# Performance work log

Measured on AMD Instinct MI355X. Metric: run time of the kernel, lower is better.

The kernel has to match this reference:

```python
import jax, jax.numpy as jnp
import numpy as np

EMBED = 1024
HEADS = 16
HEAD_DIM = EMBED // HEADS


def setup_inputs() -> dict:
    key = jax.random.key(0)
    ks = jax.random.split(key, 11)
    B, L, E = 2, 2048, EMBED
    s = 1.0 / np.sqrt(E)
    return {
        "query": jax.random.normal(ks[0], (B, L, E), jnp.float32),
        "key": jax.random.normal(ks[1], (B, L, E), jnp.float32),
        "value": jax.random.normal(ks[2], (B, L, E), jnp.float32),
        "Wq": jax.random.normal(ks[3], (E, E), jnp.float32) * s,
        "bq": jax.random.normal(ks[4], (E,), jnp.float32) * s,
        "Wk": jax.random.normal(ks[5], (E, E), jnp.float32) * s,
        "bk": jax.random.normal(ks[6], (E,), jnp.float32) * s,
        "Wv": jax.random.normal(ks[7], (E, E), jnp.float32) * s,
        "bv": jax.random.normal(ks[8], (E,), jnp.float32) * s,
        "Wo": jax.random.normal(ks[9], (E, E), jnp.float32) * s,
        "bo": jax.random.normal(ks[10], (E,), jnp.float32) * s,
    }


def reference(query, key, value, Wq, bq, Wk, bk, Wv, bv, Wo, bo):
    B, Lq, E = query.shape
    Lk = key.shape[1]
    # Linear projections (torch Linear: x @ W.T + b)
    q = (query @ Wq.T + bq).reshape(B, Lq, HEADS, HEAD_DIM).transpose(0, 2, 1, 3)
    k = (key @ Wk.T + bk).reshape(B, Lk, HEADS, HEAD_DIM).transpose(0, 2, 1, 3)
    v = (value @ Wv.T + bv).reshape(B, Lk, HEADS, HEAD_DIM).transpose(0, 2, 1, 3)
    # NOTE: original scales by sqrt(embed_size), not sqrt(head_dim)
    energy = jnp.einsum("bhqd,bhkd->bhqk", q, k) / jnp.sqrt(jnp.float32(E))
    attn = jax.nn.softmax(energy, axis=-1)
    out = jnp.einsum("bhqk,bhkd->bhqd", attn, v)  # [B,H,Lq,D]
    out = out.transpose(0, 2, 1, 3).reshape(B, Lq, E)
    return out @ Wo.T + bo
```

## Files before the change

kernel.cpp:

```cpp
#include <hip/hip_runtime.h>
#include <hip/hip_bf16.h>


typedef __attribute__((ext_vector_type(4))) float f32x4;
typedef __attribute__((ext_vector_type(16))) float f32x16;
typedef __attribute__((ext_vector_type(8))) short bf16x8;
typedef __attribute__((ext_vector_type(4))) short bf16x4;
typedef __attribute__((ext_vector_type(2))) unsigned int u32x2;

static __device__ __forceinline__ unsigned short f2bf(float f) {
  union { float f; unsigned int u; } a; a.f = f;
  unsigned int u = a.u;
  u += 0x7FFFu + ((u >> 16) & 1u);
  return (unsigned short)(u >> 16);
}

static __device__ __forceinline__ unsigned pack2(float lo, float hi) {
  unsigned a = __float_as_uint(lo) + 0x8000u;
  unsigned b = __float_as_uint(hi) + 0x8000u;
  return __builtin_amdgcn_perm(b, a, 0x07060302);
}

static __device__ __forceinline__ unsigned xchg32(unsigned x) {
  u32x2 r = __builtin_amdgcn_permlane32_swap(x, x, false, false);
  return x ^ r[0] ^ r[1];
}

#define AS1(p) ((const __attribute__((address_space(1))) void*)(p))
#define AS3(p) ((__attribute__((address_space(3))) void*)(p))

__global__ __launch_bounds__(256) void cvt_kernel(
    const float* __restrict__ q, const float* __restrict__ k, const float* __restrict__ v,
    const float* __restrict__ wq, const float* __restrict__ wk, const float* __restrict__ wv,
    const float* __restrict__ wo, short* __restrict__ ws) {
  long i = (long)blockIdx.x * 256 + threadIdx.x;
  long e = i * 8;
  const float* src; long off;
  if (e < 12582912) {
    int s = (int)(e >> 22);
    src = s == 0 ? q : (s == 1 ? k : v);
    off = e & 4194303;
  } else {
    long e2 = e - 12582912;
    int s = (int)(e2 >> 20);
    src = s == 0 ? wq : (s == 1 ? wk : (s == 2 ? wv : wo));
    off = e2 & 1048575;
  }
  f32x4 a = *(const f32x4*)(src + off);
  f32x4 b = *(const f32x4*)(src + off + 4);
  bf16x8 o;
  o[0] = (short)f2bf(a[0]); o[1] = (short)f2bf(a[1]);
  o[2] = (short)f2bf(a[2]); o[3] = (short)f2bf(a[3]);
  o[4] = (short)f2bf(b[0]); o[5] = (short)f2bf(b[1]);
  o[6] = (short)f2bf(b[2]); o[7] = (short)f2bf(b[3]);
  *(bf16x8*)(ws + e) = o;
}

__device__ __forceinline__ void gemm_tile(const short* __restrict__ A, const short* __restrict__ B,
                                          int m0, int n0, f32x4 acc[4][4],
                                          short* As, short* Bs) {
  const int t = threadIdx.x;
  const int lane = t & 63, w = t >> 6;
  const int wr = w >> 1, wc = w & 1;
  const int x = lane & 15, g = lane >> 4;
  const int lr = lane >> 3;
  const int lc = ((lane & 7) ^ lr) * 8;
  const int rswz = (x & 7) * 8;

#pragma unroll
  for (int fm = 0; fm < 4; fm++)
#pragma unroll
    for (int fn = 0; fn < 4; fn++)
#pragma unroll
      for (int r = 0; r < 4; r++) acc[fm][fn][r] = 0.0f;

  for (int k0 = 0; k0 < 1024; k0 += 64) {
    __syncthreads();
#pragma unroll
    for (int i = 0; i < 4; i++) {
      int ch = w * 4 + i;
      const short* ga = A + (long)(m0 + ch * 8 + lr) * 1024 + k0 + lc;
      __builtin_amdgcn_global_load_lds(AS1(ga), AS3(As + ch * 512), 16, 0, 0);
      const short* gb = B + (long)(n0 + ch * 8 + lr) * 1024 + k0 + lc;
      __builtin_amdgcn_global_load_lds(AS1(gb), AS3(Bs + ch * 512), 16, 0, 0);
    }
    __syncthreads();
#pragma unroll
    for (int ks = 0; ks < 2; ks++) {
      bf16x8 af[4], bfv[4];
#pragma unroll
      for (int f = 0; f < 4; f++) {
        int c = (ks * 32 + g * 8) ^ rswz;
        af[f]  = *(const bf16x8*)(As + (wr * 64 + f * 16 + x) * 64 + c);
        bfv[f] = *(const bf16x8*)(Bs + (wc * 64 + f * 16 + x) * 64 + c);
      }
#pragma unroll
      for (int fm = 0; fm < 4; fm++)
#pragma unroll
        for (int fn = 0; fn < 4; fn++)
          acc[fm][fn] = __builtin_amdgcn_mfma_f32_16x16x32_bf16(af[fm], bfv[fn], acc[fm][fn], 0, 0, 0);
    }
  }
}

__global__ __launch_bounds__(256) void proj_kernel(
    const short* __restrict__ Xq, const short* __restrict__ Xk, const short* __restrict__ Xv,
    const short* __restrict__ Wq, const short* __restrict__ Wk, const short* __restrict__ Wv,
    const float* __restrict__ bq, const float* __restrict__ bk, const float* __restrict__ bv,
    short* __restrict__ Qo, short* __restrict__ Ko, short* __restrict__ Vto) {
  __shared__ short As[8192], Bs[8192];
  const int lin = blockIdx.z * 256 + blockIdx.y * 8 + blockIdx.x;
  const int wgid = (lin & 7) * 96 + (lin >> 3);
  const int z = wgid >> 8;
  const int m0 = ((wgid >> 3) & 31) * 128, n0 = (wgid & 7) * 128;
  const short* A = z == 0 ? Xq : (z == 1 ? Xk : Xv);
  const short* B = z == 0 ? Wq : (z == 1 ? Wk : Wv);
  const float* bias = z == 0 ? bq : (z == 1 ? bk : bv);
  f32x4 acc[4][4];
  gemm_tile(A, B, m0, n0, acc, As, Bs);

  const int lane = threadIdx.x & 63, w = threadIdx.x >> 6;
  const int wr = w >> 1, wc = w & 1, x = lane & 15, g = lane >> 4;

  if (z == 0) {
    const float scale = 0.04508422002778f;
#pragma unroll
    for (int fn = 0; fn < 4; fn++) {
      int n = n0 + wc * 64 + fn * 16 + x;
      float bb = bias[n];
      int h = n >> 6, d = n & 63;
#pragma unroll
      for (int fm = 0; fm < 4; fm++) {
        int mb = m0 + wr * 64 + fm * 16 + g * 4;
#pragma unroll
        for (int r = 0; r < 4; r++) {
          int m = mb + r;
          int b = m >> 11, l = m & 2047;
          float val = (acc[fm][fn][r] + bb) * scale;
          Qo[((long)((b * 16 + h) * 2048 + l)) * 64 + d] = (short)f2bf(val);
        }
      }
    }
  } else if (z == 1) {
#pragma unroll
    for (int fn = 0; fn < 4; fn++) {
      int n = n0 + wc * 64 + fn * 16 + x;
      float bb = bias[n];
      int h = n >> 6, d = n & 63;
#pragma unroll
      for (int fm = 0; fm < 4; fm++) {
        int mb = m0 + wr * 64 + fm * 16 + g * 4;
#pragma unroll
        for (int r = 0; r < 4; r++) {
          int m = mb + r;
          int b = m >> 11, kv = m & 2047;
          int ds = d ^ ((kv & 7) << 3);
          Ko[((long)((b * 16 + h) * 2048 + kv)) * 64 + ds] = (short)f2bf(acc[fm][fn][r] + bb);
        }
      }
    }
  } else {
#pragma unroll
    for (int fn = 0; fn < 4; fn++) {
      int n = n0 + wc * 64 + fn * 16 + x;
      float bb = bias[n];
      int h = n >> 6, d = n & 63;
#pragma unroll
      for (int fm = 0; fm < 4; fm++) {
        int mb = m0 + wr * 64 + fm * 16 + g * 4;
        int b = mb >> 11, kvb = mb & 2047;
        bf16x4 pk;
#pragma unroll
        for (int r = 0; r < 4; r++) pk[r] = (short)f2bf(acc[fm][fn][r] + bb);
        int kvs = (kvb & ~63) | ((kvb & 63) ^ ((d & 7) << 3));
        *(bf16x4*)(Vto + ((long)((b * 16 + h) * 64 + d)) * 2048 + kvs) = pk;
      }
    }
  }
}

__global__ __launch_bounds__(256, 2) void attn_kernel(
    const short* __restrict__ Qg, const short* __restrict__ Kg,
    const short* __restrict__ Vtg, short* __restrict__ Og) {
  __shared__ __align__(16) short Kl[2][8192];
  __shared__ __align__(16) short Vl[2][8192];
  const int t = threadIdx.x, w = t >> 6, lane = t & 63;
  const int col = lane & 31, hi = lane >> 5;
  const int lin = blockIdx.y * 16 + blockIdx.x;
  const int wgid = (lin & 7) * 64 + (lin >> 3);
  const int bh = wgid >> 4;
  const int q0 = (wgid & 15) * 128 + w * 32;
  const long hb = (long)bh * 2048 * 64;
  const int swz = (col & 7) * 8;

  bf16x8 qf[4];
#pragma unroll
  for (int ksl = 0; ksl < 4; ksl++)
    qf[ksl] = *(const bf16x8*)(Qg + hb + (long)(q0 + col) * 64 + ksl * 16 + hi * 8);

  f32x16 o0, o1;
#pragma unroll
  for (int i = 0; i < 16; i++) { o0[i] = 0.0f; o1[i] = 0.0f; }
  float l_r = 0.0f;

  auto stage = [&](int buf, int kv0) {
#pragma unroll
    for (int it = 0; it < 4; it++) {
      int cb = it * 256 + w * 64;
      const short* gk = Kg + hb + (long)kv0 * 64 + (cb + lane) * 8;
      __builtin_amdgcn_global_load_lds(AS1(gk), AS3(&Kl[buf][cb * 8]), 16, 0, 0);
      int c = cb + lane;
      const short* gv = Vtg + hb + (long)(c >> 4) * 2048 + kv0 + (c & 15) * 8;
      __builtin_amdgcn_global_load_lds(AS1(gv), AS3(&Vl[buf][cb * 8]), 16, 0, 0);
    }
  };

  stage(0, 0);
  __syncthreads();

  for (int ti = 0; ti < 16; ti++) {
    const int buf = ti & 1;
    if (ti < 15) stage(buf ^ 1, (ti + 1) * 128);

#pragma unroll
    for (int st = 0; st < 2; st++) {
      f32x16 s0, s1;
#pragma unroll
      for (int i = 0; i < 16; i++) { s0[i] = 0.0f; s1[i] = 0.0f; }
      __builtin_amdgcn_s_setprio(1);
#pragma unroll
      for (int ksl = 0; ksl < 4; ksl++) {
        int dcol = (ksl * 16 + hi * 8) ^ swz;
        bf16x8 a0 = *(const bf16x8*)(&Kl[buf][(st * 64 + col) * 64 + dcol]);
        bf16x8 a1 = *(const bf16x8*)(&Kl[buf][(st * 64 + col + 32) * 64 + dcol]);
        s0 = __builtin_amdgcn_mfma_f32_32x32x16_bf16(a0, qf[ksl], s0, 0, 0, 0);
        s1 = __builtin_amdgcn_mfma_f32_32x32x16_bf16(a1, qf[ksl], s1, 0, 0, 0);
      }
      __builtin_amdgcn_s_setprio(0);

#pragma unroll
      for (int i = 0; i < 16; i++) { s0[i] = __builtin_amdgcn_exp2f(s0[i]); }
#pragma unroll
      for (int i = 0; i < 16; i++) { s1[i] = __builtin_amdgcn_exp2f(s1[i]); }
      {
        float a0 = s0[0] + s0[1], a1 = s0[2] + s0[3], a2 = s0[4] + s0[5], a3 = s0[6] + s0[7];
        float a4 = s0[8] + s0[9], a5 = s0[10] + s0[11], a6 = s0[12] + s0[13], a7 = s0[14] + s0[15];
        float b0 = s1[0] + s1[1], b1 = s1[2] + s1[3], b2 = s1[4] + s1[5], b3 = s1[6] + s1[7];
        float b4 = s1[8] + s1[9], b5 = s1[10] + s1[11], b6 = s1[12] + s1[13], b7 = s1[14] + s1[15];
        float c0 = a0 + a1, c1 = a2 + a3, c2 = a4 + a5, c3 = a6 + a7;
        float c4 = b0 + b1, c5 = b2 + b3, c6 = b4 + b5, c7 = b6 + b7;
        float d0 = c0 + c1, d1 = c2 + c3, d2 = c4 + c5, d3 = c6 + c7;
        l_r += (d0 + d1) + (d2 + d3);
      }

#define PVSTEP(SEL, KS)                                                       \
      {                                                                       \
        unsigned pkA0 = pack2(SEL[8 * ((KS) & 1) + 0], SEL[8 * ((KS) & 1) + 1]); \
        unsigned pkA1 = pack2(SEL[8 * ((KS) & 1) + 2], SEL[8 * ((KS) & 1) + 3]); \
        unsigned pkB0 = pack2(SEL[8 * ((KS) & 1) + 4], SEL[8 * ((KS) & 1) + 5]); \
        unsigned pkB1 = pack2(SEL[8 * ((KS) & 1) + 6], SEL[8 * ((KS) & 1) + 7]); \
        unsigned own0 = hi ? pkB0 : pkA0, own1 = hi ? pkB1 : pkA1;            \
        unsigned oth0 = hi ? pkA0 : pkB0, oth1 = hi ? pkA1 : pkB1;            \
        unsigned r0 = xchg32(oth0);                                           \
        unsigned r1 = xchg32(oth1);                                           \
        union { unsigned u[4]; bf16x8 v; } pb;                                \
        pb.u[0] = hi ? r0 : own0; pb.u[1] = hi ? r1 : own1;                   \
        pb.u[2] = hi ? own0 : r0; pb.u[3] = hi ? own1 : r1;                   \
        const int vcol = ((KS) * 16 + hi * 8) ^ swz;                          \
        bf16x8 vb0 = *(const bf16x8*)(&Vl[buf][col * 128 + st * 64 + vcol]);  \
        bf16x8 vb1 = *(const bf16x8*)(&Vl[buf][(col + 32) * 128 + st * 64 + vcol]); \
        __builtin_amdgcn_s_setprio(1);                                        \
        o0 = __builtin_amdgcn_mfma_f32_32x32x16_bf16(vb0, pb.v, o0, 0, 0, 0); \
        o1 = __builtin_amdgcn_mfma_f32_32x32x16_bf16(vb1, pb.v, o1, 0, 0, 0); \
        __builtin_amdgcn_s_setprio(0);                                        \
      }
      PVSTEP(s0, 0)
      PVSTEP(s0, 1)
      PVSTEP(s1, 2)
      PVSTEP(s1, 3)
#undef PVSTEP
    }

    __syncthreads();
  }

  const float l_tot = l_r + __uint_as_float(xchg32(__float_as_uint(l_r)));
  const float inv = 1.0f / l_tot;
  const int b = bh >> 4, h = bh & 15;
  const long base = ((long)(b * 2048 + q0 + col) * 16 + h) * 64;
#pragma unroll
  for (int dh = 0; dh < 2; dh++) {
#pragma unroll
    for (int g2 = 0; g2 < 4; g2++) {
      float x0 = (dh ? o1[g2 * 4 + 0] : o0[g2 * 4 + 0]) * inv;
      float x1 = (dh ? o1[g2 * 4 + 1] : o0[g2 * 4 + 1]) * inv;
      float x2 = (dh ? o1[g2 * 4 + 2] : o0[g2 * 4 + 2]) * inv;
      float x3 = (dh ? o1[g2 * 4 + 3] : o0[g2 * 4 + 3]) * inv;
      u32x2 rr;
      rr[0] = (unsigned)f2bf(x0) | ((unsigned)f2bf(x1) << 16);
      rr[1] = (unsigned)f2bf(x2) | ((unsigned)f2bf(x3) << 16);
      int d = dh * 32 + g2 * 8 + hi * 4;
      *(u32x2*)(Og + base + d) = rr;
    }
  }
}

__global__ __launch_bounds__(256) void out_kernel(
    const short* __restrict__ O, const short* __restrict__ Wo,
    const float* __restrict__ bo, float* __restrict__ out) {
  __shared__ short As[8192], Bs[8192];
  const int lin = blockIdx.y * 8 + blockIdx.x;
  const int wgid = (lin & 7) * 32 + (lin >> 3);
  const int m0 = (wgid >> 3) * 128, n0 = (wgid & 7) * 128;
  f32x4 acc[4][4];
  gemm_tile(O, Wo, m0, n0, acc, As, Bs);
  const int lane = threadIdx.x & 63, w = threadIdx.x >> 6;
  const int wr = w >> 1, wc = w & 1, x = lane & 15, g = lane >> 4;
#pragma unroll
  for (int fn = 0; fn < 4; fn++) {
    int n = n0 + wc * 64 + fn * 16 + x;
    float bb = bo[n];
#pragma unroll
    for (int fm = 0; fm < 4; fm++) {
      int mb = m0 + wr * 64 + fm * 16 + g * 4;
#pragma unroll
      for (int r = 0; r < 4; r++)
        out[(long)(mb + r) * 1024 + n] = acc[fm][fn][r] + bb;
    }
  }
}

extern "C" void kernel_launch(void* const* d_in, const int* in_sizes, int n_in,
                              void* d_out, int out_size, void* d_ws, size_t ws_size,
                              hipStream_t stream) {
  const float* q  = (const float*)d_in[0];
  const float* k  = (const float*)d_in[1];
  const float* v  = (const float*)d_in[2];
  const float* wq = (const float*)d_in[3];
  const float* bq = (const float*)d_in[4];
  const float* wk = (const float*)d_in[5];
  const float* bk = (const float*)d_in[6];
  const float* wv = (const float*)d_in[7];
  const float* bv = (const float*)d_in[8];
  const float* wo = (const float*)d_in[9];
  const float* bo = (const float*)d_in[10];

  short* ws  = (short*)d_ws;
  short* Xq  = ws;
  short* Xk  = Xq + 4194304;
  short* Xv  = Xk + 4194304;
  short* Wqb = Xv + 4194304;
  short* Wkb = Wqb + 1048576;
  short* Wvb = Wkb + 1048576;
  short* Wob = Wvb + 1048576;
  short* Qb  = Wob + 1048576;
  short* Kb  = Qb + 4194304;
  short* Vtb = Kb + 4194304;
  short* Ob  = Vtb + 4194304;

  cvt_kernel<<<8192, 256, 0, stream>>>(q, k, v, wq, wk, wv, wo, ws);
  dim3 gp(8, 32, 3);
  proj_kernel<<<gp, 256, 0, stream>>>(Xq, Xk, Xv, Wqb, Wkb, Wvb, bq, bk, bv, Qb, Kb, Vtb);
  dim3 ga(16, 32);
  attn_kernel<<<ga, 256, 0, stream>>>(Qb, Kb, Vtb, Ob);
  dim3 gf(8, 32);
  out_kernel<<<gf, 256, 0, stream>>>(Ob, Wob, bo, (float*)d_out);
}
```

Baseline: 130.3 us.

## Fuse activation bf16 conversion into projection GEMM and compute row sums via MFMA

The separate conversion pass for the query/key/value activations is removed. The projection GEMM now loads fp32 activations directly, packs them to bf16 in registers and writes them to LDS, which avoids a full write and reread of the activation tensors. In attention, the scalar softmax row-sum reduction is replaced by an extra MFMA against a ones vector that accumulates the denominator. This adds matrix-core work per step and gives up the async global-to-LDS path for the A operand.

Result: no change. 131.8 us (+1.1%).

```diff
diff --git a/kernel.cpp b/kernel.cpp
--- a/kernel.cpp
+++ b/kernel.cpp
@@ -29,23 +29,15 @@
 #define AS1(p) ((const __attribute__((address_space(1))) void*)(p))
 #define AS3(p) ((__attribute__((address_space(3))) void*)(p))
 
-__global__ __launch_bounds__(256) void cvt_kernel(
-    const float* __restrict__ q, const float* __restrict__ k, const float* __restrict__ v,
-    const float* __restrict__ wq, const float* __restrict__ wk, const float* __restrict__ wv,
-    const float* __restrict__ wo, short* __restrict__ ws) {
+__global__ __launch_bounds__(256) void cvtw_kernel(
+    const float* __restrict__ wq, const float* __restrict__ wk,
+    const float* __restrict__ wv, const float* __restrict__ wo,
+    short* __restrict__ ws) {
   long i = (long)blockIdx.x * 256 + threadIdx.x;
   long e = i * 8;
-  const float* src; long off;
-  if (e < 12582912) {
-    int s = (int)(e >> 22);
-    src = s == 0 ? q : (s == 1 ? k : v);
-    off = e & 4194303;
-  } else {
-    long e2 = e - 12582912;
-    int s = (int)(e2 >> 20);
-    src = s == 0 ? wq : (s == 1 ? wk : (s == 2 ? wv : wo));
-    off = e2 & 1048575;
-  }
+  int s = (int)(e >> 20);
+  const float* src = s == 0 ? wq : (s == 1 ? wk : (s == 2 ? wv : wo));
+  long off = e & 1048575;
   f32x4 a = *(const f32x4*)(src + off);
   f32x4 b = *(const f32x4*)(src + off + 4);
   bf16x8 o;
@@ -103,8 +95,69 @@
   }
 }
 
+__device__ __forceinline__ void gemm_tile_f32a(const float* __restrict__ A,
+                                               const short* __restrict__ B,
+                                               int m0, int n0, f32x4 acc[4][4],
+                                               short* As, short* Bs) {
+  const int t = threadIdx.x;
+  const int lane = t & 63, w = t >> 6;
+  const int wr = w >> 1, wc = w & 1;
+  const int x = lane & 15, g = lane >> 4;
+  const int lr = lane >> 3;
+  const int sc = (lane & 7) * 8;
+  const int dcA = sc ^ (lr * 8);
+  const int lcB = ((lane & 7) ^ lr) * 8;
+  const int rswz = (x & 7) * 8;
+
+#pragma unroll
+  for (int fm = 0; fm < 4; fm++)
+#pragma unroll
+    for (int fn = 0; fn < 4; fn++)
+#pragma unroll
+      for (int r = 0; r < 4; r++) acc[fm][fn][r] = 0.0f;
+
+  for (int k0 = 0; k0 < 1024; k0 += 64) {
+    __syncthreads();
+#pragma unroll
+    for (int i = 0; i < 4; i++) {
+      int ch = w * 4 + i;
+      const short* gb = B + (long)(n0 + ch * 8 + lr) * 1024 + k0 + lcB;
+      __builtin_amdgcn_global_load_lds(AS1(gb), AS3(Bs + ch * 512), 16, 0, 0);
+    }
+#pragma unroll
+    for (int i = 0; i < 4; i++) {
+      int ch = w * 4 + i;
+      const float* ga = A + (long)(m0 + ch * 8 + lr) * 1024 + k0 + sc;
+      f32x4 a = *(const f32x4*)ga;
+      f32x4 b2 = *(const f32x4*)(ga + 4);
+      union { unsigned u[4]; bf16x8 v; } pk;
+      pk.u[0] = pack2(a[0], a[1]);
+      pk.u[1] = pack2(a[2], a[3]);
+      pk.u[2] = pack2(b2[0], b2[1]);
+      pk.u[3] = pack2(b2[2], b2[3]);
+      *(bf16x8*)(As + (ch * 8 + lr) * 64 + dcA) = pk.v;
+    }
+    __syncthreads();
+#pragma unroll
+    for (int ks = 0; ks < 2; ks++) {
+      bf16x8 af[4], bfv[4];
+#pragma unroll
+      for (int f = 0; f < 4; f++) {
+        int c = (ks * 32 + g * 8) ^ rswz;
+        af[f]  = *(const bf16x8*)(As + (wr * 64 + f * 16 + x) * 64 + c);
+        bfv[f] = *(const bf16x8*)(Bs + (wc * 64 + f * 16 + x) * 64 + c);
+      }
+#pragma unroll
+      for (int fm = 0; fm < 4; fm++)
+#pragma unroll
+        for (int fn = 0; fn < 4; fn++)
+          acc[fm][fn] = __builtin_amdgcn_mfma_f32_16x16x32_bf16(af[fm], bfv[fn], acc[fm][fn], 0, 0, 0);
+    }
+  }
+}
+
 __global__ __launch_bounds__(256) void proj_kernel(
-    const short* __restrict__ Xq, const short* __restrict__ Xk, const short* __restrict__ Xv,
+    const float* __restrict__ Xq, const float* __restrict__ Xk, const float* __restrict__ Xv,
     const short* __restrict__ Wq, const short* __restrict__ Wk, const short* __restrict__ Wv,
     const float* __restrict__ bq, const float* __restrict__ bk, const float* __restrict__ bv,
     short* __restrict__ Qo, short* __restrict__ Ko, short* __restrict__ Vto) {
@@ -113,11 +166,11 @@
   const int wgid = (lin & 7) * 96 + (lin >> 3);
   const int z = wgid >> 8;
   const int m0 = ((wgid >> 3) & 31) * 128, n0 = (wgid & 7) * 128;
-  const short* A = z == 0 ? Xq : (z == 1 ? Xk : Xv);
+  const float* A = z == 0 ? Xq : (z == 1 ? Xk : Xv);
   const short* B = z == 0 ? Wq : (z == 1 ? Wk : Wv);
   const float* bias = z == 0 ? bq : (z == 1 ? bk : bv);
   f32x4 acc[4][4];
-  gemm_tile(A, B, m0, n0, acc, As, Bs);
+  gemm_tile_f32a(A, B, m0, n0, acc, As, Bs);
 
   const int lane = threadIdx.x & 63, w = threadIdx.x >> 6;
   const int wr = w >> 1, wc = w & 1, x = lane & 15, g = lane >> 4;
@@ -198,10 +251,13 @@
   for (int ksl = 0; ksl < 4; ksl++)
     qf[ksl] = *(const bf16x8*)(Qg + hb + (long)(q0 + col) * 64 + ksl * 16 + hi * 8);
 
-  f32x16 o0, o1;
-#pragma unroll
-  for (int i = 0; i < 16; i++) { o0[i] = 0.0f; o1[i] = 0.0f; }
-  float l_r = 0.0f;
+  union { unsigned u[4]; bf16x8 v; } onesf;
+#pragma unroll
+  for (int i = 0; i < 4; i++) onesf.u[i] = 0x3F803F80u;
+
+  f32x16 o0, o1, o2;
+#pragma unroll
+  for (int i = 0; i < 16; i++) { o0[i] = 0.0f; o1[i] = 0.0f; o2[i] = 0.0f; }
 
   auto stage = [&](int buf, int kv0) {
 #pragma unroll
@@ -242,16 +298,6 @@
       for (int i = 0; i < 16; i++) { s0[i] = __builtin_amdgcn_exp2f(s0[i]); }
 #pragma unroll
       for (int i = 0; i < 16; i++) { s1[i] = __builtin_amdgcn_exp2f(s1[i]); }
-      {
-        float a0 = s0[0] + s0[1], a1 = s0[2] + s0[3], a2 = s0[4] + s0[5], a3 = s0[6] + s0[7];
-        float a4 = s0[8] + s0[9], a5 = s0[10] + s0[11], a6 = s0[12] + s0[13], a7 = s0[14] + s0[15];
-        float b0 = s1[0] + s1[1], b1 = s1[2] + s1[3], b2 = s1[4] + s1[5], b3 = s1[6] + s1[7];
-        float b4 = s1[8] + s1[9], b5 = s1[10] + s1[11], b6 = s1[12] + s1[13], b7 = s1[14] + s1[15];
-        float c0 = a0 + a1, c1 = a2 + a3, c2 = a4 + a5, c3 = a6 + a7;
-        float c4 = b0 + b1, c5 = b2 + b3, c6 = b4 + b5, c7 = b6 + b7;
-        float d0 = c0 + c1, d1 = c2 + c3, d2 = c4 + c5, d3 = c6 + c7;
-        l_r += (d0 + d1) + (d2 + d3);
-      }
 
 #define PVSTEP(SEL, KS)                                                       \
       {                                                                       \
@@ -272,6 +318,7 @@
         __builtin_amdgcn_s_setprio(1);                                        \
         o0 = __builtin_amdgcn_mfma_f32_32x32x16_bf16(vb0, pb.v, o0, 0, 0, 0); \
         o1 = __builtin_amdgcn_mfma_f32_32x32x16_bf16(vb1, pb.v, o1, 0, 0, 0); \
+        o2 = __builtin_amdgcn_mfma_f32_32x32x16_bf16(onesf.v, pb.v, o2, 0, 0, 0); \
         __builtin_amdgcn_s_setprio(0);                                        \
       }
       PVSTEP(s0, 0)
@@ -284,8 +331,7 @@
     __syncthreads();
   }
 
-  const float l_tot = l_r + __uint_as_float(xchg32(__float_as_uint(l_r)));
-  const float inv = 1.0f / l_tot;
+  const float inv = 1.0f / o2[0];
   const int b = bh >> 4, h = bh & 15;
   const long base = ((long)(b * 2048 + q0 + col) * 16 + h) * 64;
 #pragma unroll
@@ -346,10 +392,7 @@
   const float* bo = (const float*)d_in[10];
 
   short* ws  = (short*)d_ws;
-  short* Xq  = ws;
-  short* Xk  = Xq + 4194304;
-  short* Xv  = Xk + 4194304;
-  short* Wqb = Xv + 4194304;
+  short* Wqb = ws;
   short* Wkb = Wqb + 1048576;
   short* Wvb = Wkb + 1048576;
   short* Wob = Wvb + 1048576;
@@ -358,9 +401,9 @@
   short* Vtb = Kb + 4194304;
   short* Ob  = Vtb + 4194304;
 
-  cvt_kernel<<<8192, 256, 0, stream>>>(q, k, v, wq, wk, wv, wo, ws);
+  cvtw_kernel<<<2048, 256, 0, stream>>>(wq, wk, wv, wo, ws);
   dim3 gp(8, 32, 3);
-  proj_kernel<<<gp, 256, 0, stream>>>(Xq, Xk, Xv, Wqb, Wkb, Wvb, bq, bk, bv, Qb, Kb, Vtb);
+  proj_kernel<<<gp, 256, 0, stream>>>(q, k, v, Wqb, Wkb, Wvb, bq, bk, bv, Qb, Kb, Vtb);
   dim3 ga(16, 32);
   attn_kernel<<<ga, 256, 0, stream>>>(Qb, Kb, Vtb, Ob);
   dim3 gf(8, 32);
```
